# Performance work log

Hardware: AMD Instinct MI355X
Metric: run time of the kernel (lower is better)

Reference implementation:

```python
import math
import jax, jax.numpy as jnp
import numpy as np

B, T, D = 128, 243, 1024   # batch, motion frames, latent_dim
N, L = 77, 512             # text tokens, text_latent_dim
H = 16                     # num_head -> head_dim 64
EPS = 1e-5


def _ln(x, g, b):
    m = x.mean(-1, keepdims=True)
    v = jnp.var(x, axis=-1, keepdims=True)
    return (x - m) * jax.lax.rsqrt(v + EPS) * g + b


def setup_inputs() -> dict:
    key = jax.random.key(0)
    ks = jax.random.split(key, 16)
    s = 0.02
    return {
        "x": jax.random.normal(ks[0], (B, T, D), jnp.float32),
        "xf": jax.random.normal(ks[1], (B, N, L), jnp.float32),
        "emb": jax.random.normal(ks[2], (B, T, D), jnp.float32),
        "ln_g": jnp.ones((D,), jnp.float32), "ln_b": jnp.zeros((D,), jnp.float32),
        "tln_g": jnp.ones((L,), jnp.float32), "tln_b": jnp.zeros((L,), jnp.float32),
        "Wq": jax.random.normal(ks[3], (D, D), jnp.float32) * s,
        "bq": jnp.zeros((D,), jnp.float32),
        "Wk": jax.random.normal(ks[4], (L, D), jnp.float32) * s,
        "bk": jnp.zeros((D,), jnp.float32),
        "Wv": jax.random.normal(ks[5], (L, D), jnp.float32) * s,
        "bv": jnp.zeros((D,), jnp.float32),
        "We": jax.random.normal(ks[6], (D, 2 * D), jnp.float32) * s,  # emb_layers Linear(time_embed_dim=D, 2D)
        "be": jnp.zeros((2 * D,), jnp.float32),
        "ln2_g": jnp.ones((D,), jnp.float32), "ln2_b": jnp.zeros((D,), jnp.float32),
        "Wo": jax.random.normal(ks[7], (D, D), jnp.float32) * s,     # zero_module in torch; random here for non-trivial baseline
        "bo": jnp.zeros((D,), jnp.float32),
    }


def reference(x, xf, emb, ln_g, ln_b, tln_g, tln_b, Wq, bq, Wk, bk, Wv, bv,
              We, be, ln2_g, ln2_b, Wo, bo):
    B_, T_, D_ = x.shape
    dh = D_ // H
    # cross-attention: queries from motion tokens, keys/values from text
    q = (_ln(x, ln_g, ln_b) @ Wq + bq).reshape(B_, T_, H, dh)
    xfn = _ln(xf, tln_g, tln_b)
    k = (xfn @ Wk + bk).reshape(B_, -1, H, dh)
    v = (xfn @ Wv + bv).reshape(B_, -1, H, dh)
    att = jnp.einsum('bthd,bnhd->btnh', q, k) / math.sqrt(dh)  # (B,T,N,H)
    w = jax.nn.softmax(att, axis=2)                            # softmax over text tokens; dropout is eval-mode identity
    y = jnp.einsum('btnh,bnhd->bthd', w, v).reshape(B_, T_, D_)
    # StylizationBlock (AdaLN): emb viewed (B,T,D), only first timestep used
    emb_out = (jax.nn.silu(emb) @ We + be)[:, 0:1, :]          # (B,1,2D)
    scale, shift = jnp.split(emb_out, 2, axis=2)
    h = _ln(y, ln2_g, ln2_b) * (1.0 + scale) + shift
    h = jax.nn.silu(h) @ Wo + bo
    return x + h
```

## Files before the change

kernel.cpp:

```cpp
#include <hip/hip_runtime.h>
#include <cstdint>

typedef __attribute__((ext_vector_type(8))) __bf16 bf16x8;
typedef __attribute__((ext_vector_type(4))) float f32x4;
typedef __attribute__((ext_vector_type(8))) unsigned short ushort8v;

__device__ __forceinline__ float b2f(unsigned short u) {
    union { uint32_t i; float f; } w; w.i = ((uint32_t)u) << 16; return w.f;
}
__device__ __forceinline__ unsigned short f2b(float f) {
    union { uint32_t i; float f; } w; w.f = f;
    uint32_t r = (w.i + 0x7FFFu + ((w.i >> 16) & 1u)) >> 16;
    return (unsigned short)r;
}

__device__ __forceinline__ void gl16(const unsigned short* g, unsigned short* l) {
    __builtin_amdgcn_global_load_lds(
        (const __attribute__((address_space(1))) void*)g,
        (__attribute__((address_space(3))) void*)l,
        16, 0, 0);
}

__device__ __forceinline__ int swz8(int wg, int nwg) {
    const int q = nwg >> 3, r = nwg & 7;
    const int xcd = wg & 7, idx = wg >> 3;
    return (xcd < r) ? (xcd * (q + 1) + idx)
                     : (r * (q + 1) + (xcd - r) * q + idx);
}

__global__ __launch_bounds__(256) void k_cvt_all(
    const float* __restrict__ Wq, const float* __restrict__ Wk,
    const float* __restrict__ Wv, const float* __restrict__ We,
    const float* __restrict__ Wo,
    unsigned short* __restrict__ wqt, unsigned short* __restrict__ wkvt,
    unsigned short* __restrict__ wet, unsigned short* __restrict__ wot) {
    __shared__ float s[32][33];
    int bid = blockIdx.x;
    const float* in; unsigned short* out; int R, C;
    if (bid < 1024)      { in = Wq; out = wqt;              R = 1024; C = 1024; }
    else if (bid < 1536) { bid -= 1024; in = Wk; out = wkvt;             R = 512;  C = 1024; }
    else if (bid < 2048) { bid -= 1536; in = Wv; out = wkvt + 1024 * 512; R = 512;  C = 1024; }
    else if (bid < 4096) { bid -= 2048; in = We; out = wet;              R = 1024; C = 2048; }
    else                 { bid -= 4096; in = Wo; out = wot;              R = 1024; C = 1024; }
    const int ctiles = C >> 5;
    const int c0 = (bid % ctiles) * 32, r0 = (bid / ctiles) * 32;
    const int tx = threadIdx.x & 31, ty = threadIdx.x >> 5;
#pragma unroll
    for (int i = 0; i < 4; ++i)
        s[ty + i * 8][tx] = in[(size_t)(r0 + ty + i * 8) * C + c0 + tx];
    __syncthreads();
#pragma unroll
    for (int i = 0; i < 4; ++i)
        out[(size_t)(c0 + ty + i * 8) * R + r0 + tx] = f2b(s[tx][ty + i * 8]);
}

template <int DIM>
__global__ __launch_bounds__(256) void k_ln(const float* __restrict__ in,
                                            const float* __restrict__ g,
                                            const float* __restrict__ b,
                                            unsigned short* __restrict__ out) {
    const int row = blockIdx.x * 4 + (threadIdx.x >> 6);
    const int ln = threadIdx.x & 63;
    constexpr int PL = DIM / 64;
    float v[PL];
    const size_t base = (size_t)row * DIM + (size_t)ln * PL;
    const float4* p4 = (const float4*)(in + base);
#pragma unroll
    for (int c = 0; c < PL / 4; ++c) {
        const float4 t = p4[c];
        v[c * 4 + 0] = t.x; v[c * 4 + 1] = t.y; v[c * 4 + 2] = t.z; v[c * 4 + 3] = t.w;
    }
    float s = 0.f, s2 = 0.f;
#pragma unroll
    for (int c = 0; c < PL; ++c) { s += v[c]; s2 += v[c] * v[c]; }
    for (int o = 1; o < 64; o <<= 1) { s += __shfl_xor(s, o); s2 += __shfl_xor(s2, o); }
    const float mean = s / DIM;
    const float rstd = rsqrtf(s2 / DIM - mean * mean + 1e-5f);
    const float4* g4 = (const float4*)(g + ln * PL);
    const float4* b4 = (const float4*)(b + ln * PL);
#pragma unroll
    for (int c0 = 0; c0 < PL; c0 += 8) {
        ushort8v yv;
#pragma unroll
        for (int j = 0; j < 8; ++j) {
            const int c = c0 + j;
            const float gg = ((const float*)g4)[c];
            const float bb = ((const float*)b4)[c];
            yv[j] = f2b((v[c] - mean) * rstd * gg + bb);
        }
        *(ushort8v*)(out + base + c0) = yv;
    }
}

__global__ __launch_bounds__(256) void k_silu(const float* __restrict__ emb,
                                              unsigned short* __restrict__ se) {
    const int i = blockIdx.x * 256 + threadIdx.x;
    const int b = i >> 10, k = i & 1023;
    const float f = emb[(size_t)b * (243 * 1024) + k];
    se[i] = f2b(f / (1.f + __expf(-f)));
}

__device__ __forceinline__ void mm_body(
    int u, int NN,
    const unsigned short* __restrict__ A, const unsigned short* __restrict__ Bt,
    const float* __restrict__ bias0, const float* __restrict__ bias1,
    unsigned short* __restrict__ C0, unsigned short* __restrict__ C1,
    float* __restrict__ Cf, const float* __restrict__ X,
    int N, int K, int epi,
    unsigned short* sA, unsigned short* sB) {
    const int tid = threadIdx.x, wv = tid >> 6, ln = tid & 63;
    const int wm = wv >> 2, wn = wv & 3;
    const int ln15 = ln & 15, lg = ln >> 4;
    const int m0 = (u / NN) * 128, n0 = (u % NN) * 256;

    const f32x4 fz = {0.f, 0.f, 0.f, 0.f};
    f32x4 acc[4][4];
#pragma unroll
    for (int i = 0; i < 4; ++i)
#pragma unroll
        for (int j = 0; j < 4; ++j) acc[i][j] = fz;

    const int lrow = ln >> 3;
    const int sslot = (ln & 7) ^ lrow;
    const unsigned short* ga = A + (size_t)(m0 + wv * 16 + lrow) * K + sslot * 8;
    const unsigned short* gb = Bt + (size_t)(n0 + wv * 32 + lrow) * K + sslot * 8;
    unsigned short* const lA = sA + (wv * 16) * 64;
    unsigned short* const lB = sB + (wv * 32) * 64;

    for (int k0 = 0; k0 < K; k0 += 64) {
#pragma unroll
        for (int i = 0; i < 2; ++i)
            gl16(ga + k0 + (size_t)i * 8 * K, lA + i * 8 * 64);
#pragma unroll
        for (int i = 0; i < 4; ++i)
            gl16(gb + k0 + (size_t)i * 8 * K, lB + i * 8 * 64);
        __syncthreads();
        bf16x8 af[4][2], bf[4][2];
#pragma unroll
        for (int i = 0; i < 4; ++i) {
            const int ra2 = wm * 64 + i * 16 + ln15;
            const int rb2 = wn * 64 + i * 16 + ln15;
#pragma unroll
            for (int ks = 0; ks < 2; ++ks) {
                const int slot = ks * 4 + lg;
                af[i][ks] = *(const bf16x8*)(sA + ra2 * 64 + ((slot ^ (ra2 & 7)) * 8));
                bf[i][ks] = *(const bf16x8*)(sB + rb2 * 64 + ((slot ^ (rb2 & 7)) * 8));
            }
        }
#pragma unroll
        for (int mi = 0; mi < 4; ++mi)
#pragma unroll
            for (int ni = 0; ni < 4; ++ni) {
                acc[mi][ni] = __builtin_amdgcn_mfma_f32_16x16x32_bf16(af[mi][0], bf[ni][0], acc[mi][ni], 0, 0, 0);
                acc[mi][ni] = __builtin_amdgcn_mfma_f32_16x16x32_bf16(af[mi][1], bf[ni][1], acc[mi][ni], 0, 0, 0);
            }
        __syncthreads();
    }

    const int colB = n0 + wn * 64;
    const int rowB = m0 + wm * 64;
#pragma unroll
    for (int mi = 0; mi < 4; ++mi) {
#pragma unroll
        for (int ni = 0; ni < 4; ++ni) {
            const int col = colB + ni * 16 + ln15;
            const int row = rowB + mi * 16 + lg * 4;
            float bvv;
            if (epi == 2) bvv = (col < 1024) ? bias0[col] : bias1[col - 1024];
            else bvv = bias0[col];
#pragma unroll
            for (int r2 = 0; r2 < 4; ++r2) {
                const float v = acc[mi][ni][r2] + bvv;
                if (epi == 0) {
                    C0[(size_t)(row + r2) * N + col] = f2b(v);
                } else if (epi == 1) {
                    Cf[(size_t)(row + r2) * N + col] = v + X[(size_t)(row + r2) * N + col];
                } else if (epi == 2) {
                    if (col < 1024) C0[(size_t)(row + r2) * 1024 + col] = f2b(v);
                    else C1[(size_t)(row + r2) * 1024 + (col - 1024)] = f2b(v);
                } else {
                    Cf[(size_t)(row + r2) * N + col] = v;
                }
            }
        }
    }
}

__global__ __launch_bounds__(512, 2) void k_mm3(
    const unsigned short* __restrict__ xn, const unsigned short* __restrict__ wqt,
    const float* __restrict__ bq, unsigned short* __restrict__ qb,
    const unsigned short* __restrict__ xfn, const unsigned short* __restrict__ wkvt,
    const float* __restrict__ bk, const float* __restrict__ bv,
    unsigned short* __restrict__ kb, unsigned short* __restrict__ vb,
    const unsigned short* __restrict__ se, const unsigned short* __restrict__ wet,
    const float* __restrict__ be, float* __restrict__ eo) {
    __shared__ __align__(16) unsigned short sA[128 * 64];
    __shared__ __align__(16) unsigned short sB[256 * 64];
    const int wg = blockIdx.x;
    if (wg < 972) {
        mm_body(swz8(wg, 972), 4, xn, wqt, bq, nullptr, qb, nullptr, nullptr, nullptr,
                1024, 1024, 0, sA, sB);
    } else if (wg < 1588) {
        mm_body(swz8(wg - 972, 616), 8, xfn, wkvt, bk, bv, kb, vb, nullptr, nullptr,
                2048, 512, 2, sA, sB);
    } else {
        mm_body(wg - 1588, 8, se, wet, be, nullptr, nullptr, nullptr, eo, nullptr,
                2048, 1024, 3, sA, sB);
    }
}

__global__ __launch_bounds__(512, 2) void k_mm1(
    const unsigned short* __restrict__ actb, const unsigned short* __restrict__ wot,
    const float* __restrict__ bo, const float* __restrict__ x,
    float* __restrict__ outp) {
    __shared__ __align__(16) unsigned short sA[128 * 64];
    __shared__ __align__(16) unsigned short sB[256 * 64];
    mm_body(swz8(blockIdx.x, 972), 4, actb, wot, bo, nullptr, nullptr, nullptr,
            outp, x, 1024, 1024, 1, sA, sB);
}

__global__ __launch_bounds__(256, 2) void k_attn_m(const unsigned short* __restrict__ Q,
                                                   const unsigned short* __restrict__ Kb,
                                                   const unsigned short* __restrict__ Vb,
                                                   unsigned short* __restrict__ Y) {
    __shared__ __align__(16) unsigned short sK[80 * 64];
    __shared__ __align__(16) unsigned short sVr[80 * 72];
    __shared__ __align__(16) unsigned short sV[64 * 96];
    __shared__ __align__(16) unsigned short sP[4][16 * 104];
    const int bh = blockIdx.x;
    const int b = bh >> 4, h = bh & 15;
    const int tid = threadIdx.x, wv = tid >> 6, ln = tid & 63;
    const int ln15 = ln & 15, lg = ln >> 4;

    for (int c = tid; c < 640; c += 256) {
        const int n = c >> 3, ci = c & 7;
        uint4 kv = make_uint4(0u, 0u, 0u, 0u), vv = make_uint4(0u, 0u, 0u, 0u);
        if (n < 77) {
            const size_t o = (size_t)(b * 77 + n) * 1024 + h * 64 + ci * 8;
            kv = *(const uint4*)(Kb + o);
            vv = *(const uint4*)(Vb + o);
        }
        *(uint4*)((char*)sK + n * 128 + ((ci * 16) ^ ((n & 7) << 4))) = kv;
        *(uint4*)(sVr + n * 72 + ci * 8) = vv;
    }
    bf16x8 qf[4][2];
    const size_t qbase = (size_t)b * (243 * 1024) + h * 64;
#pragma unroll
    for (int mi = 0; mi < 4; ++mi) {
        int t = wv * 64 + mi * 16 + ln15;
        if (t > 242) t = 242;
#pragma unroll
        for (int ks = 0; ks < 2; ++ks)
            qf[mi][ks] = *(const bf16x8*)(Q + qbase + (size_t)t * 1024 + ks * 32 + lg * 8);
    }
    __syncthreads();

    for (int i = tid; i < 64 * 96; i += 256) {
        const int d = i / 96, n = i - d * 96;
        sV[i] = (n < 80) ? sVr[n * 72 + d] : (unsigned short)0;
    }
    for (int i = ln; i < 16 * 24; i += 64) {
        const int rr = i / 24, cc = i - rr * 24;
        sP[wv][rr * 104 + 80 + cc] = 0;
    }
    __syncthreads();

    const f32x4 fz = {0.f, 0.f, 0.f, 0.f};
#pragma unroll
    for (int mi = 0; mi < 4; ++mi) {
        f32x4 sc[5];
#pragma unroll
        for (int ci = 0; ci < 5; ++ci) sc[ci] = fz;
#pragma unroll
        for (int ci = 0; ci < 5; ++ci) {
            const int n = ci * 16 + ln15;
#pragma unroll
            for (int ks = 0; ks < 2; ++ks) {
                const int kk = ks * 32 + lg * 8;
                bf16x8 kf = *(const bf16x8*)((const char*)sK + n * 128 + ((kk * 2) ^ ((n & 7) << 4)));
                sc[ci] = __builtin_amdgcn_mfma_f32_16x16x32_bf16(qf[mi][ks], kf, sc[ci], 0, 0, 0);
            }
        }
#pragma unroll
        for (int r = 0; r < 4; ++r) {
            float e[5];
            float mx = -1e30f;
#pragma unroll
            for (int ci = 0; ci < 5; ++ci) {
                const int n = ci * 16 + ln15;
                const float vv = (n < 77) ? sc[ci][r] * 0.125f : -1e30f;
                e[ci] = vv;
                mx = fmaxf(mx, vv);
            }
            mx = fmaxf(mx, __shfl_xor(mx, 1));
            mx = fmaxf(mx, __shfl_xor(mx, 2));
            mx = fmaxf(mx, __shfl_xor(mx, 4));
            mx = fmaxf(mx, __shfl_xor(mx, 8));
            float ssum = 0.f;
#pragma unroll
            for (int ci = 0; ci < 5; ++ci) {
                const int n = ci * 16 + ln15;
                const float ev = (n < 77) ? __expf(e[ci] - mx) : 0.f;
                e[ci] = ev;
                ssum += ev;
            }
            ssum += __shfl_xor(ssum, 1);
            ssum += __shfl_xor(ssum, 2);
            ssum += __shfl_xor(ssum, 4);
            ssum += __shfl_xor(ssum, 8);
            const float inv = 1.f / ssum;
            const int prow = lg * 4 + r;
#pragma unroll
            for (int ci = 0; ci < 5; ++ci)
                sP[wv][prow * 104 + ci * 16 + ln15] = f2b(e[ci] * inv);
        }
        f32x4 ya[4];
#pragma unroll
        for (int di = 0; di < 4; ++di) ya[di] = fz;
#pragma unroll
        for (int ks = 0; ks < 3; ++ks) {
            bf16x8 pa = *(const bf16x8*)(sP[wv] + ln15 * 104 + ks * 32 + lg * 8);
#pragma unroll
            for (int di = 0; di < 4; ++di) {
                bf16x8 vf = *(const bf16x8*)(sV + (di * 16 + ln15) * 96 + ks * 32 + lg * 8);
                ya[di] = __builtin_amdgcn_mfma_f32_16x16x32_bf16(pa, vf, ya[di], 0, 0, 0);
            }
        }
        unsigned short* sy = sP[wv];
#pragma unroll
        for (int di = 0; di < 4; ++di)
#pragma unroll
            for (int r = 0; r < 4; ++r)
                sy[(lg * 4 + r) * 72 + di * 16 + ln15] = f2b(ya[di][r]);
        const int tb = wv * 64 + mi * 16;
#pragma unroll
        for (int j = 0; j < 2; ++j) {
            const int k = ln * 2 + j;
            const int row = k >> 3, off = (k & 7) * 8;
            const int t = tb + row;
            if (t < 243)
                *(uint4*)(Y + qbase + (size_t)t * 1024 + off) = *(const uint4*)(sy + row * 72 + off);
        }
    }
}

__global__ __launch_bounds__(256) void k_act(const unsigned short* __restrict__ y,
                                             const float* __restrict__ eo,
                                             const float* __restrict__ g,
                                             const float* __restrict__ b,
                                             unsigned short* __restrict__ out) {
    const int row = blockIdx.x * 4 + (threadIdx.x >> 6);
    const int ln = threadIdx.x & 63;
    const int bb = row / 243;
    float v[16];
    const size_t base = (size_t)row * 1024 + ln * 16;
#pragma unroll
    for (int c0 = 0; c0 < 16; c0 += 8) {
        const ushort8v t = *(const ushort8v*)(y + base + c0);
#pragma unroll
        for (int j = 0; j < 8; ++j) v[c0 + j] = b2f(t[j]);
    }
    float s = 0.f, s2 = 0.f;
#pragma unroll
    for (int c = 0; c < 16; ++c) { s += v[c]; s2 += v[c] * v[c]; }
    for (int o = 1; o < 64; o <<= 1) { s += __shfl_xor(s, o); s2 += __shfl_xor(s2, o); }
    const float mean = s / 1024.f;
    const float rstd = rsqrtf(s2 / 1024.f - mean * mean + 1e-5f);
    const float* gp = g + ln * 16;
    const float* bp = b + ln * 16;
    const float* sc = eo + (size_t)bb * 2048 + ln * 16;
    const float* sh = sc + 1024;
#pragma unroll
    for (int c0 = 0; c0 < 16; c0 += 8) {
        ushort8v yv;
#pragma unroll
        for (int j = 0; j < 8; ++j) {
            const int c = c0 + j;
            const float nl = (v[c] - mean) * rstd * gp[c] + bp[c];
            const float hh = nl * (1.f + sc[c]) + sh[c];
            yv[j] = f2b(hh / (1.f + __expf(-hh)));
        }
        *(ushort8v*)(out + base + c0) = yv;
    }
}

extern "C" void kernel_launch(void* const* d_in, const int* in_sizes, int n_in,
                              void* d_out, int out_size, void* d_ws, size_t ws_size,
                              hipStream_t stream) {
    (void)in_sizes; (void)n_in; (void)out_size; (void)ws_size;

    const float* x     = (const float*)d_in[0];
    const float* xf    = (const float*)d_in[1];
    const float* emb   = (const float*)d_in[2];
    const float* ln_g  = (const float*)d_in[3];
    const float* ln_b  = (const float*)d_in[4];
    const float* tln_g = (const float*)d_in[5];
    const float* tln_b = (const float*)d_in[6];
    const float* Wq    = (const float*)d_in[7];
    const float* bq    = (const float*)d_in[8];
    const float* Wk    = (const float*)d_in[9];
    const float* bk    = (const float*)d_in[10];
    const float* Wv    = (const float*)d_in[11];
    const float* bv    = (const float*)d_in[12];
    const float* We    = (const float*)d_in[13];
    const float* be    = (const float*)d_in[14];
    const float* ln2_g = (const float*)d_in[15];
    const float* ln2_b = (const float*)d_in[16];
    const float* Wo    = (const float*)d_in[17];
    const float* bo    = (const float*)d_in[18];
    float* outp = (float*)d_out;

    char* ws = (char*)d_ws;
    constexpr size_t o_wq   = 0;
    constexpr size_t o_wkv  = o_wq + 2097152;
    constexpr size_t o_we   = o_wkv + 2097152;
    constexpr size_t o_wo   = o_we + 4194304;
    constexpr size_t o_se   = o_wo + 2097152;
    constexpr size_t o_eo   = o_se + 262144;
    constexpr size_t o_xn   = o_eo + 1048576;
    constexpr size_t o_qb   = o_xn + 63700992;
    constexpr size_t o_xfn  = o_qb + 63700992;
    constexpr size_t o_kb   = o_xfn + 10092544;
    constexpr size_t o_vb   = o_kb + 20185088;

    unsigned short* wqt  = (unsigned short*)(ws + o_wq);
    unsigned short* wkvt = (unsigned short*)(ws + o_wkv);
    unsigned short* wet  = (unsigned short*)(ws + o_we);
    unsigned short* wot  = (unsigned short*)(ws + o_wo);
    unsigned short* se   = (unsigned short*)(ws + o_se);
    float*          eo   = (float*)(ws + o_eo);
    unsigned short* xn   = (unsigned short*)(ws + o_xn);
    unsigned short* yb   = xn;
    unsigned short* qb   = (unsigned short*)(ws + o_qb);
    unsigned short* actb = qb;
    unsigned short* xfn  = (unsigned short*)(ws + o_xfn);
    unsigned short* kb   = (unsigned short*)(ws + o_kb);
    unsigned short* vb   = (unsigned short*)(ws + o_vb);

    k_ln<1024><<<7776, 256, 0, stream>>>(x, ln_g, ln_b, xn);
    k_ln<512><<<2464, 256, 0, stream>>>(xf, tln_g, tln_b, xfn);
    k_silu<<<512, 256, 0, stream>>>(emb, se);
    k_cvt_all<<<5120, 256, 0, stream>>>(Wq, Wk, Wv, We, Wo, wqt, wkvt, wet, wot);

    k_mm3<<<1596, 512, 0, stream>>>(xn, wqt, bq, qb,
                                    xfn, wkvt, bk, bv, kb, vb,
                                    se, wet, be, eo);

    k_attn_m<<<2048, 256, 0, stream>>>(qb, kb, vb, yb);

    k_act<<<7776, 256, 0, stream>>>(yb, eo, ln2_g, ln2_b, actb);

    k_mm1<<<972, 512, 0, stream>>>(actb, wot, bo, x, outp);
}
```

Baseline: 353.5 us.

## Shrink GEMM tiles to 128x128 and merge preprocessing kernels into one launch

The GEMM body now uses 128x128 output tiles instead of 128x256. Each wave computes a 32x64 sub-tile with half the accumulators, and the grids double. The intent is better load balance and occupancy across the CUs, at the cost of lower arithmetic intensity and more A-tile re-reads. Separately, the two LayerNorm kernels, SiLU and the weight conversion are fused into a single k_pre launch to cut launch overhead and the gaps between kernels.

```diff
diff --git a/kernel.cpp b/kernel.cpp
--- a/kernel.cpp
+++ b/kernel.cpp
@@ -28,7 +28,48 @@
                      : (r * (q + 1) + (xcd - r) * q + idx);
 }
 
-__global__ __launch_bounds__(256) void k_cvt_all(
+template <int DIM>
+__device__ __forceinline__ void ln_body(int bid, const float* __restrict__ in,
+                                        const float* __restrict__ g,
+                                        const float* __restrict__ b,
+                                        unsigned short* __restrict__ out) {
+    const int row = bid * 4 + (threadIdx.x >> 6);
+    const int ln = threadIdx.x & 63;
+    constexpr int PL = DIM / 64;
+    float v[PL];
+    const size_t base = (size_t)row * DIM + (size_t)ln * PL;
+    const float4* p4 = (const float4*)(in + base);
+#pragma unroll
+    for (int c = 0; c < PL / 4; ++c) {
+        const float4 t = p4[c];
+        v[c * 4 + 0] = t.x; v[c * 4 + 1] = t.y; v[c * 4 + 2] = t.z; v[c * 4 + 3] = t.w;
+    }
+    float s = 0.f, s2 = 0.f;
+#pragma unroll
+    for (int c = 0; c < PL; ++c) { s += v[c]; s2 += v[c] * v[c]; }
+    for (int o = 1; o < 64; o <<= 1) { s += __shfl_xor(s, o); s2 += __shfl_xor(s2, o); }
+    const float mean = s / DIM;
+    const float rstd = rsqrtf(s2 / DIM - mean * mean + 1e-5f);
+    const float* gp = g + ln * PL;
+    const float* bp = b + ln * PL;
+#pragma unroll
+    for (int c0 = 0; c0 < PL; c0 += 8) {
+        ushort8v yv;
+#pragma unroll
+        for (int j = 0; j < 8; ++j) {
+            const int c = c0 + j;
+            yv[j] = f2b((v[c] - mean) * rstd * gp[c] + bp[c]);
+        }
+        *(ushort8v*)(out + base + c0) = yv;
+    }
+}
+
+__global__ __launch_bounds__(256) void k_pre(
+    const float* __restrict__ x, const float* __restrict__ ln_g, const float* __restrict__ ln_b,
+    unsigned short* __restrict__ xn,
+    const float* __restrict__ xf, const float* __restrict__ tln_g, const float* __restrict__ tln_b,
+    unsigned short* __restrict__ xfn,
+    const float* __restrict__ emb, unsigned short* __restrict__ se,
     const float* __restrict__ Wq, const float* __restrict__ Wk,
     const float* __restrict__ Wv, const float* __restrict__ We,
     const float* __restrict__ Wo,
@@ -36,6 +77,18 @@
     unsigned short* __restrict__ wet, unsigned short* __restrict__ wot) {
     __shared__ float s[32][33];
     int bid = blockIdx.x;
+    if (bid < 7776) { ln_body<1024>(bid, x, ln_g, ln_b, xn); return; }
+    bid -= 7776;
+    if (bid < 2464) { ln_body<512>(bid, xf, tln_g, tln_b, xfn); return; }
+    bid -= 2464;
+    if (bid < 512) {
+        const int i = bid * 256 + threadIdx.x;
+        const int b = i >> 10, k = i & 1023;
+        const float f = emb[(size_t)b * (243 * 1024) + k];
+        se[i] = f2b(f / (1.f + __expf(-f)));
+        return;
+    }
+    bid -= 512;
     const float* in; unsigned short* out; int R, C;
     if (bid < 1024)      { in = Wq; out = wqt;              R = 1024; C = 1024; }
     else if (bid < 1536) { bid -= 1024; in = Wk; out = wkvt;             R = 512;  C = 1024; }
@@ -54,52 +107,6 @@
         out[(size_t)(c0 + ty + i * 8) * R + r0 + tx] = f2b(s[tx][ty + i * 8]);
 }
 
-template <int DIM>
-__global__ __launch_bounds__(256) void k_ln(const float* __restrict__ in,
-                                            const float* __restrict__ g,
-                                            const float* __restrict__ b,
-                                            unsigned short* __restrict__ out) {
-    const int row = blockIdx.x * 4 + (threadIdx.x >> 6);
-    const int ln = threadIdx.x & 63;
-    constexpr int PL = DIM / 64;
-    float v[PL];
-    const size_t base = (size_t)row * DIM + (size_t)ln * PL;
-    const float4* p4 = (const float4*)(in + base);
-#pragma unroll
-    for (int c = 0; c < PL / 4; ++c) {
-        const float4 t = p4[c];
-        v[c * 4 + 0] = t.x; v[c * 4 + 1] = t.y; v[c * 4 + 2] = t.z; v[c * 4 + 3] = t.w;
-    }
-    float s = 0.f, s2 = 0.f;
-#pragma unroll
-    for (int c = 0; c < PL; ++c) { s += v[c]; s2 += v[c] * v[c]; }
-    for (int o = 1; o < 64; o <<= 1) { s += __shfl_xor(s, o); s2 += __shfl_xor(s2, o); }
-    const float mean = s / DIM;
-    const float rstd = rsqrtf(s2 / DIM - mean * mean + 1e-5f);
-    const float4* g4 = (const float4*)(g + ln * PL);
-    const float4* b4 = (const float4*)(b + ln * PL);
-#pragma unroll
-    for (int c0 = 0; c0 < PL; c0 += 8) {
-        ushort8v yv;
-#pragma unroll
-        for (int j = 0; j < 8; ++j) {
-            const int c = c0 + j;
-            const float gg = ((const float*)g4)[c];
-            const float bb = ((const float*)b4)[c];
-            yv[j] = f2b((v[c] - mean) * rstd * gg + bb);
-        }
-        *(ushort8v*)(out + base + c0) = yv;
-    }
-}
-
-__global__ __launch_bounds__(256) void k_silu(const float* __restrict__ emb,
-                                              unsigned short* __restrict__ se) {
-    const int i = blockIdx.x * 256 + threadIdx.x;
-    const int b = i >> 10, k = i & 1023;
-    const float f = emb[(size_t)b * (243 * 1024) + k];
-    se[i] = f2b(f / (1.f + __expf(-f)));
-}
-
 __device__ __forceinline__ void mm_body(
     int u, int NN,
     const unsigned short* __restrict__ A, const unsigned short* __restrict__ Bt,
@@ -109,46 +116,52 @@
     int N, int K, int epi,
     unsigned short* sA, unsigned short* sB) {
     const int tid = threadIdx.x, wv = tid >> 6, ln = tid & 63;
-    const int wm = wv >> 2, wn = wv & 3;
+    const int wm = wv >> 1, wn = wv & 1;
     const int ln15 = ln & 15, lg = ln >> 4;
-    const int m0 = (u / NN) * 128, n0 = (u % NN) * 256;
+    const int m0 = (u / NN) * 128, n0 = (u % NN) * 128;
 
     const f32x4 fz = {0.f, 0.f, 0.f, 0.f};
-    f32x4 acc[4][4];
-#pragma unroll
-    for (int i = 0; i < 4; ++i)
+    f32x4 acc[2][4];
+#pragma unroll
+    for (int i = 0; i < 2; ++i)
 #pragma unroll
         for (int j = 0; j < 4; ++j) acc[i][j] = fz;
 
     const int lrow = ln >> 3;
     const int sslot = (ln & 7) ^ lrow;
     const unsigned short* ga = A + (size_t)(m0 + wv * 16 + lrow) * K + sslot * 8;
-    const unsigned short* gb = Bt + (size_t)(n0 + wv * 32 + lrow) * K + sslot * 8;
+    const unsigned short* gb = Bt + (size_t)(n0 + wv * 16 + lrow) * K + sslot * 8;
     unsigned short* const lA = sA + (wv * 16) * 64;
-    unsigned short* const lB = sB + (wv * 32) * 64;
+    unsigned short* const lB = sB + (wv * 16) * 64;
 
     for (int k0 = 0; k0 < K; k0 += 64) {
 #pragma unroll
-        for (int i = 0; i < 2; ++i)
+        for (int i = 0; i < 2; ++i) {
             gl16(ga + k0 + (size_t)i * 8 * K, lA + i * 8 * 64);
-#pragma unroll
-        for (int i = 0; i < 4; ++i)
             gl16(gb + k0 + (size_t)i * 8 * K, lB + i * 8 * 64);
+        }
         __syncthreads();
-        bf16x8 af[4][2], bf[4][2];
-#pragma unroll
-        for (int i = 0; i < 4; ++i) {
-            const int ra2 = wm * 64 + i * 16 + ln15;
-            const int rb2 = wn * 64 + i * 16 + ln15;
+        bf16x8 af[2][2], bf[4][2];
+#pragma unroll
+        for (int i = 0; i < 2; ++i) {
+            const int ra2 = wm * 32 + i * 16 + ln15;
 #pragma unroll
             for (int ks = 0; ks < 2; ++ks) {
                 const int slot = ks * 4 + lg;
                 af[i][ks] = *(const bf16x8*)(sA + ra2 * 64 + ((slot ^ (ra2 & 7)) * 8));
+            }
+        }
+#pragma unroll
+        for (int i = 0; i < 4; ++i) {
+            const int rb2 = wn * 64 + i * 16 + ln15;
+#pragma unroll
+            for (int ks = 0; ks < 2; ++ks) {
+                const int slot = ks * 4 + lg;
                 bf[i][ks] = *(const bf16x8*)(sB + rb2 * 64 + ((slot ^ (rb2 & 7)) * 8));
             }
         }
 #pragma unroll
-        for (int mi = 0; mi < 4; ++mi)
+        for (int mi = 0; mi < 2; ++mi)
 #pragma unroll
             for (int ni = 0; ni < 4; ++ni) {
                 acc[mi][ni] = __builtin_amdgcn_mfma_f32_16x16x32_bf16(af[mi][0], bf[ni][0], acc[mi][ni], 0, 0, 0);
@@ -158,9 +171,9 @@
     }
 
     const int colB = n0 + wn * 64;
-    const int rowB = m0 + wm * 64;
-#pragma unroll
-    for (int mi = 0; mi < 4; ++mi) {
+    const int rowB = m0 + wm * 32;
+#pragma unroll
+    for (int mi = 0; mi < 2; ++mi) {
 #pragma unroll
         for (int ni = 0; ni < 4; ++ni) {
             const int col = colB + ni * 16 + ln15;
@@ -195,16 +208,16 @@
     const unsigned short* __restrict__ se, const unsigned short* __restrict__ wet,
     const float* __restrict__ be, float* __restrict__ eo) {
     __shared__ __align__(16) unsigned short sA[128 * 64];
-    __shared__ __align__(16) unsigned short sB[256 * 64];
+    __shared__ __align__(16) unsigned short sB[128 * 64];
     const int wg = blockIdx.x;
-    if (wg < 972) {
-        mm_body(swz8(wg, 972), 4, xn, wqt, bq, nullptr, qb, nullptr, nullptr, nullptr,
+    if (wg < 1944) {
+        mm_body(swz8(wg, 1944), 8, xn, wqt, bq, nullptr, qb, nullptr, nullptr, nullptr,
                 1024, 1024, 0, sA, sB);
-    } else if (wg < 1588) {
-        mm_body(swz8(wg - 972, 616), 8, xfn, wkvt, bk, bv, kb, vb, nullptr, nullptr,
+    } else if (wg < 3176) {
+        mm_body(swz8(wg - 1944, 1232), 16, xfn, wkvt, bk, bv, kb, vb, nullptr, nullptr,
                 2048, 512, 2, sA, sB);
     } else {
-        mm_body(wg - 1588, 8, se, wet, be, nullptr, nullptr, nullptr, eo, nullptr,
+        mm_body(wg - 3176, 16, se, wet, be, nullptr, nullptr, nullptr, eo, nullptr,
                 2048, 1024, 3, sA, sB);
     }
 }
@@ -214,8 +227,8 @@
     const float* __restrict__ bo, const float* __restrict__ x,
     float* __restrict__ outp) {
     __shared__ __align__(16) unsigned short sA[128 * 64];
-    __shared__ __align__(16) unsigned short sB[256 * 64];
-    mm_body(swz8(blockIdx.x, 972), 4, actb, wot, bo, nullptr, nullptr, nullptr,
+    __shared__ __align__(16) unsigned short sB[128 * 64];
+    mm_body(swz8(blockIdx.x, 1944), 8, actb, wot, bo, nullptr, nullptr, nullptr,
             outp, x, 1024, 1024, 1, sA, sB);
 }
 
@@ -437,12 +450,13 @@
     unsigned short* kb   = (unsigned short*)(ws + o_kb);
     unsigned short* vb   = (unsigned short*)(ws + o_vb);
 
-    k_ln<1024><<<7776, 256, 0, stream>>>(x, ln_g, ln_b, xn);
-    k_ln<512><<<2464, 256, 0, stream>>>(xf, tln_g, tln_b, xfn);
-    k_silu<<<512, 256, 0, stream>>>(emb, se);
-    k_cvt_all<<<5120, 256, 0, stream>>>(Wq, Wk, Wv, We, Wo, wqt, wkvt, wet, wot);
-
-    k_mm3<<<1596, 512, 0, stream>>>(xn, wqt, bq, qb,
+    k_pre<<<15872, 256, 0, stream>>>(x, ln_g, ln_b, xn,
+                                     xf, tln_g, tln_b, xfn,
+                                     emb, se,
+                                     Wq, Wk, Wv, We, Wo,
+                                     wqt, wkvt, wet, wot);
+
+    k_mm3<<<3192, 512, 0, stream>>>(xn, wqt, bq, qb,
                                     xfn, wkvt, bk, bv, kb, vb,
                                     se, wet, be, eo);
 
@@ -450,5 +464,5 @@
 
     k_act<<<7776, 256, 0, stream>>>(yb, eo, ln2_g, ln2_b, actb);
 
-    k_mm1<<<972, 512, 0, stream>>>(actb, wot, bo, x, outp);
-}
+    k_mm1<<<1944, 512, 0, stream>>>(actb, wot, bo, x, outp);
+}
```

Measured after the change: 359.2 us. About the same (+1.6%).
